# Kernel tuning notes

Measured on AMD Instinct MI355X. Metric: run time of the kernel, lower is better.

## Reference

```python
import jax, jax.numpy as jnp
import numpy as np

B, S_ENC, T_DEC, I, H = 1024, 49, 25, 76, 2048  # S_ENC = source_seq_len - 1


def setup_inputs() -> dict:
    key = jax.random.key(0)
    ks = jax.random.split(key, 6)
    sc = 0.02
    return {
        "encoder_inputs": jax.random.normal(ks[0], (B, S_ENC, I), jnp.float32),
        "decoder_inputs": jax.random.normal(ks[1], (B, T_DEC, I), jnp.float32),
        "W_ih": jax.random.normal(ks[2], (3 * H, I), jnp.float32) * sc,
        "W_hh": jax.random.normal(ks[3], (3 * H, H), jnp.float32) * sc,
        "b_ih": jnp.zeros((3 * H,), jnp.float32),
        "b_hh": jnp.zeros((3 * H,), jnp.float32),
        "fc_w": jax.random.normal(ks[4], (I, H), jnp.float32) * sc,
        "fc_b": jnp.zeros((I,), jnp.float32),
    }


def gru_cell(x, h, W_ih, W_hh, b_ih, b_hh):
    # PyTorch GRUCell: gates stacked [r; z; n] along first axis of weights.
    gi = x @ W_ih.T + b_ih  # [B, 3H]
    gh = h @ W_hh.T + b_hh  # [B, 3H]
    i_r, i_z, i_n = jnp.split(gi, 3, axis=-1)
    h_r, h_z, h_n = jnp.split(gh, 3, axis=-1)
    r = jax.nn.sigmoid(i_r + h_r)
    z = jax.nn.sigmoid(i_z + h_z)
    n = jnp.tanh(i_n + r * h_n)
    return (1.0 - z) * n + z * h


def reference(encoder_inputs, decoder_inputs, W_ih, W_hh, b_ih, b_hh, fc_w, fc_b):
    # Dropout p=0.0 (and eval mode) -> identity; omitted.
    h0 = jnp.zeros((encoder_inputs.shape[0], H), encoder_inputs.dtype)
    enc = jnp.swapaxes(encoder_inputs, 0, 1)  # [S_ENC, B, I]

    def enc_step(h, x):
        return gru_cell(x, h, W_ih, W_hh, b_ih, b_hh), None

    h, _ = jax.lax.scan(enc_step, h0, enc)

    # Sampling-based decoding: only decoder_inputs[:, 0] is consumed; every
    # later step feeds back the previous output. Each step's input is detached.
    prev0 = decoder_inputs[:, 0, :]

    def dec_step(carry, _):
        h, prev = carry
        inp = jax.lax.stop_gradient(prev)  # inp.detach() in the torch code
        h_new = gru_cell(inp, h, W_ih, W_hh, b_ih, b_hh)
        out = inp + h_new @ fc_w.T + fc_b  # residual over fc1 projection
        return (h_new, out), out

    _, outs = jax.lax.scan(dec_step, (h, prev0), None, length=T_DEC)
    return jnp.swapaxes(outs, 0, 1)  # [B, T_DEC, I]
```

## Files before the change

kernel.cpp:

```cpp
#include <hip/hip_runtime.h>
#include <cstdint>
#include <cstddef>

#define DI __device__ __forceinline__

typedef __bf16 bf16x8 __attribute__((ext_vector_type(8)));
typedef float  f32x4  __attribute__((ext_vector_type(4)));
typedef unsigned short ushort_t;

constexpr int BATCH = 1024;
constexpr int HID   = 2048;
constexpr int IN    = 76;
constexpr int SENC  = 49;
constexpr int TDEC  = 25;
constexpr int KX    = 128;
constexpr int KP    = KX + HID;
constexpr int BK    = 128;
constexpr int KTT   = KP / BK;
constexpr int OSTR  = TDEC * IN;

DI unsigned short f2bf(float f) {
  union { float f; unsigned u; } v; v.f = f;
  unsigned u = v.u;
  return (unsigned short)((u + 0x7fffu + ((u >> 16) & 1u)) >> 16);
}

DI float bf2f(unsigned short h) {
  union { unsigned u; float f; } v; v.u = ((unsigned)h) << 16;
  return v.f;
}

DI f32x4 mfma16(bf16x8 a, bf16x8 b, f32x4 c) {
  return __builtin_amdgcn_mfma_f32_16x16x32_bf16(a, b, c, 0, 0, 0);
}

DI void gload_lds16(const void* g, void* l) {
  __builtin_amdgcn_global_load_lds((const __attribute__((address_space(1))) void*)g,
                                   (__attribute__((address_space(3))) void*)l,
                                   16, 0, 0);
}

DI float sigmoidf_(float x) { return 1.0f / (1.0f + __expf(-x)); }
DI float tanhf_(float x)    { return 1.0f - 2.0f / (1.0f + __expf(2.0f * x)); }


__global__ void pack_W(const float* __restrict__ Wih, const float* __restrict__ Whh,
                       ushort_t* __restrict__ Wp) {
  int idx = blockIdx.x * 256 + threadIdx.x;
  if (idx >= 6144 * KP) return;
  int n = idx / KP;
  int k = idx - n * KP;
  float v = 0.f;
  if (k < IN)        v = Wih[(size_t)n * IN + k];
  else if (k >= KX)  v = Whh[(size_t)n * HID + (k - KX)];
  Wp[idx] = f2bf(v);
}

__global__ void pack_xe(const float* __restrict__ enc, ushort_t* __restrict__ xe) {
  int idx = blockIdx.x * 256 + threadIdx.x;
  if (idx >= SENC * BATCH * KX) return;
  int t = idx >> 17;
  int rem = idx & 131071;
  int b = rem >> 7, k = rem & 127;
  float v = (k < IN) ? enc[(size_t)b * (SENC * IN) + t * IN + k] : 0.f;
  xe[idx] = f2bf(v);
}

__global__ void pack_xd0(const float* __restrict__ dec, ushort_t* __restrict__ xd) {
  int idx = blockIdx.x * 256 + threadIdx.x;
  if (idx >= BATCH * KX) return;
  int b = idx >> 7, k = idx & 127;
  float v = (k < IN) ? dec[(size_t)b * OSTR + k] : 0.f;
  xd[idx] = f2bf(v);
}

__global__ void pack_fc(const float* __restrict__ fcw, ushort_t* __restrict__ Wfc) {
  int idx = blockIdx.x * 256 + threadIdx.x;
  if (idx >= 80 * HID) return;
  int n = idx >> 11, k = idx & 2047;
  float v = (n < IN) ? fcw[(size_t)n * HID + k] : 0.f;
  Wfc[idx] = f2bf(v);
}

__global__ __launch_bounds__(512, 2) void gru_step_kernel(
    const ushort_t* __restrict__ x,
    const ushort_t* __restrict__ hbp,
    const ushort_t* __restrict__ Wp,
    const float*    __restrict__ b_ih,
    const float*    __restrict__ b_hh,
    ushort_t*       __restrict__ hbn)
{
  __shared__ ushort_t lds[2][(128 + 192) * BK];

  const int tid  = threadIdx.x;
  const int lane = tid & 63;
  const int wid  = tid >> 6;
  const int bid  = blockIdx.x;
  const int n_grp = (bid & 7) + 8 * (bid >> 6);
  const int m_grp = (bid >> 3) & 7;
  const int row0  = m_grp * 128;
  const int col0  = n_grp * 64;
  const int wm = wid >> 1, wn = wid & 1;

  const f32x4 Z4 = {0.f, 0.f, 0.f, 0.f};
  f32x4 accr[2][2], accz[2][2], accin[2][2], accN[2][2];
  #pragma unroll
  for (int a = 0; a < 2; ++a)
    #pragma unroll
    for (int b = 0; b < 2; ++b) { accr[a][b] = Z4; accz[a][b] = Z4; accin[a][b] = Z4; accN[a][b] = Z4; }

  const int l15 = lane & 15;
  const int lhi = lane >> 4;

  auto stage = [&](int buf, int kt) {
    const ushort_t* asrc; int astr, ak0;
    if (kt == 0) { asrc = x;   astr = KX;  ak0 = 0; }
    else         { asrc = hbp; astr = HID; ak0 = (kt - 1) * BK; }
    ushort_t* Lb = &lds[buf][0];
    #pragma unroll
    for (int c = 0; c < 4; ++c) {
      const int chunk = wid * 4 + c;
      const int rl = chunk * 4 + lhi;
      const int swz = ((l15 ^ (((chunk & 3) << 2) + lhi)) << 3);
      const ushort_t* g = asrc + (size_t)(row0 + rl) * astr + ak0 + swz;
      gload_lds16(g, Lb + chunk * 512);
    }
    const int wk0 = kt * BK;
    #pragma unroll
    for (int c = 0; c < 6; ++c) {
      const int chunk = wid * 6 + c;
      const int brow = chunk * 4 + lhi;
      const int gg = brow >> 6, wi = brow & 63;
      const int swz = ((l15 ^ (((chunk & 3) << 2) + lhi)) << 3);
      const ushort_t* g = Wp + (size_t)(gg * HID + col0 + wi) * KP + wk0 + swz;
      gload_lds16(g, Lb + 128 * BK + chunk * 512);
    }
  };

  auto readFrags = [&](const ushort_t* base, int ks, bf16x8 af[2], bf16x8 bg[3][2]) {
    const int el = (((ks << 2) + lhi) ^ l15) << 3;
    #pragma unroll
    for (int fm = 0; fm < 2; ++fm)
      af[fm] = *reinterpret_cast<const bf16x8*>(&base[(wm * 32 + fm * 16 + l15) * BK + el]);
    #pragma unroll
    for (int g = 0; g < 3; ++g)
      #pragma unroll
      for (int fn = 0; fn < 2; ++fn)
        bg[g][fn] = *reinterpret_cast<const bf16x8*>(
            &base[128 * BK + (g * 64 + wn * 32 + fn * 16 + l15) * BK + el]);
  };

  auto burst = [&](bf16x8 af[2], bf16x8 bg[3][2]) {
    __builtin_amdgcn_s_setprio(1);
    #pragma unroll
    for (int fm = 0; fm < 2; ++fm)
      #pragma unroll
      for (int fn = 0; fn < 2; ++fn) {
        accr[fm][fn] = mfma16(af[fm], bg[0][fn], accr[fm][fn]);
        accz[fm][fn] = mfma16(af[fm], bg[1][fn], accz[fm][fn]);
        accN[fm][fn] = mfma16(af[fm], bg[2][fn], accN[fm][fn]);
      }
    __builtin_amdgcn_s_setprio(0);
  };

  bf16x8 afA[2], bgA[3][2];
  bf16x8 afB[2], bgB[3][2];

  stage(0, 0);
  asm volatile("s_waitcnt vmcnt(0)" ::: "memory");
  __builtin_amdgcn_s_barrier();
  readFrags(&lds[0][0], 0, afA, bgA);

  for (int kt = 0; kt < KTT; ++kt) {
    const ushort_t* base = &lds[kt & 1][0];
    if (kt + 1 < KTT) stage((kt + 1) & 1, kt + 1);

    readFrags(base, 1, afB, bgB);  burst(afA, bgA);
    readFrags(base, 2, afA, bgA);  burst(afB, bgB);
    readFrags(base, 3, afB, bgB);  burst(afA, bgA);
    burst(afB, bgB);

    if (kt == 0) {
      #pragma unroll
      for (int a = 0; a < 2; ++a)
        #pragma unroll
        for (int b = 0; b < 2; ++b) { accin[a][b] = accN[a][b]; accN[a][b] = Z4; }
    }

    if (kt + 1 < KTT) {
      asm volatile("s_waitcnt vmcnt(0)" ::: "memory");
      __builtin_amdgcn_s_barrier();
      readFrags(&lds[(kt + 1) & 1][0], 0, afA, bgA);
    }
  }

  const int lqb = lhi * 4;
  #pragma unroll
  for (int fn = 0; fn < 2; ++fn) {
    const int j = col0 + wn * 32 + fn * 16 + l15;
    const float br  = b_ih[j] + b_hh[j];
    const float bz  = b_ih[HID + j] + b_hh[HID + j];
    const float bin = b_ih[2 * HID + j];
    const float bhn = b_hh[2 * HID + j];
    #pragma unroll
    for (int fm = 0; fm < 2; ++fm) {
      #pragma unroll
      for (int q = 0; q < 4; ++q) {
        const int row = row0 + wm * 32 + fm * 16 + lqb + q;
        const size_t off = (size_t)row * HID + j;
        const float hp = bf2f(hbp[off]);
        const float rr = sigmoidf_(accr[fm][fn][q] + br);
        const float zz = sigmoidf_(accz[fm][fn][q] + bz);
        const float nn = tanhf_(accin[fm][fn][q] + bin + rr * (accN[fm][fn][q] + bhn));
        const float hv = (1.0f - zz) * nn + zz * hp;
        hbn[off] = f2bf(hv);
      }
    }
  }
}

__global__ __launch_bounds__(256) void fc_kernel(
    const ushort_t* __restrict__ hb,
    const ushort_t* __restrict__ Wfc,
    const float*    __restrict__ fc_b,
    const float*    __restrict__ prev,
    float*          __restrict__ outp,
    ushort_t*       __restrict__ xd)
{
  __shared__ float red[4][16][80];
  const int tid = threadIdx.x, lane = tid & 63, wid = tid >> 6;
  const int r0 = blockIdx.x * 16;
  const int lr = lane & 15, lk = (lane >> 4) * 8;
  const f32x4 Z4 = {0.f, 0.f, 0.f, 0.f};
  f32x4 acc[5];
  #pragma unroll
  for (int f = 0; f < 5; ++f) acc[f] = Z4;
  const int kbase = wid * 512;
  #pragma unroll
  for (int ks = 0; ks < 16; ++ks) {
    const int k = kbase + ks * 32 + lk;
    bf16x8 a = *reinterpret_cast<const bf16x8*>(&hb[(size_t)(r0 + lr) * HID + k]);
    #pragma unroll
    for (int f = 0; f < 5; ++f) {
      bf16x8 b = *reinterpret_cast<const bf16x8*>(&Wfc[(size_t)(f * 16 + lr) * HID + k]);
      acc[f] = mfma16(a, b, acc[f]);
    }
  }
  #pragma unroll
  for (int f = 0; f < 5; ++f)
    #pragma unroll
    for (int q = 0; q < 4; ++q)
      red[wid][(lane >> 4) * 4 + q][f * 16 + lr] = acc[f][q];
  __syncthreads();

  const int rowi = tid >> 4;
  const int j0   = (tid & 15) * 8;
  const int b_   = r0 + rowi;
  #pragma unroll
  for (int jj = 0; jj < 8; ++jj) {
    const int j = j0 + jj;
    float ov = 0.f;
    if (j < IN) {
      float s = red[0][rowi][j] + red[1][rowi][j] + red[2][rowi][j] + red[3][rowi][j];
      ov = prev[(size_t)b_ * OSTR + j] + fc_b[j] + s;
      outp[(size_t)b_ * OSTR + j] = ov;
    }
    xd[b_ * KX + j] = f2bf(j < IN ? ov : 0.f);
  }
}

extern "C" void kernel_launch(void* const* d_in, const int* in_sizes, int n_in,
                              void* d_out, int out_size, void* d_ws, size_t ws_size,
                              hipStream_t stream) {
  const float* enc = (const float*)d_in[0];
  const float* dec = (const float*)d_in[1];
  const float* Wih = (const float*)d_in[2];
  const float* Whh = (const float*)d_in[3];
  const float* bih = (const float*)d_in[4];
  const float* bhh = (const float*)d_in[5];
  const float* fcw = (const float*)d_in[6];
  const float* fcb = (const float*)d_in[7];
  float* out = (float*)d_out;

  char* ws = (char*)d_ws;
  ushort_t* Wp  = (ushort_t*)ws;  ws += (size_t)6144 * KP * 2;
  ushort_t* xe  = (ushort_t*)ws;  ws += (size_t)SENC * BATCH * KX * 2;
  ushort_t* xd  = (ushort_t*)ws;  ws += (size_t)BATCH * KX * 2;
  ushort_t* Wfc = (ushort_t*)ws;  ws += (size_t)80 * HID * 2;
  ushort_t* hb0 = (ushort_t*)ws;  ws += (size_t)BATCH * HID * 2;
  ushort_t* hb1 = (ushort_t*)ws;  ws += (size_t)BATCH * HID * 2;
  ushort_t* hbp[2] = {hb0, hb1};

  pack_W  <<<(6144 * KP + 255) / 256, 256, 0, stream>>>(Wih, Whh, Wp);
  pack_xe <<<(SENC * BATCH * KX + 255) / 256, 256, 0, stream>>>(enc, xe);
  pack_xd0<<<(BATCH * KX + 255) / 256, 256, 0, stream>>>(dec, xd);
  pack_fc <<<(80 * HID + 255) / 256, 256, 0, stream>>>(fcw, Wfc);
  hipMemsetAsync(hb0, 0, (size_t)BATCH * HID * 2, stream);

  for (int s = 0; s < SENC + TDEC; ++s) {
    const ushort_t* xsrc = (s < SENC) ? (xe + (size_t)s * BATCH * KX) : xd;
    gru_step_kernel<<<256, 512, 0, stream>>>(xsrc, hbp[s & 1], Wp, bih, bhh,
                                             hbp[(s + 1) & 1]);
    if (s >= SENC) {
      const int t = s - SENC;
      const float* prev = (t == 0) ? dec : (out + (size_t)(t - 1) * IN);
      fc_kernel<<<64, 256, 0, stream>>>(hbp[(s + 1) & 1], Wfc, fcb, prev,
                                        out + (size_t)t * IN, xd);
    }
  }
}
```

Measured before the change: 2.631 ms.

## Halve GRU block threads, double per-wave tile, deepen LDS fragment pipeline

Each GRU step block now runs 256 threads instead of 512, so every wave computes a 64x64 output sub-tile (four M fragments) rather than 32x64. The main loop is restructured into a four-stage register pipeline (A/B/C/D fragment sets), with the x-projection tile peeled out as a prologue and the next tile's global-to-LDS load issued between fragment reads. s_setprio around the MFMA bursts is removed. Intent is more MFMA work per LDS fragment read and better latency hiding. The cost is much higher register pressure (64 accumulator vectors plus four fragment sets) and fewer waves per block for hiding memory latency.

```diff
diff --git a/kernel.cpp b/kernel.cpp
--- a/kernel.cpp
+++ b/kernel.cpp
@@ -82,7 +82,7 @@
   Wfc[idx] = f2bf(v);
 }
 
-__global__ __launch_bounds__(512, 2) void gru_step_kernel(
+__global__ __launch_bounds__(256, 1) void gru_step_kernel(
     const ushort_t* __restrict__ x,
     const ushort_t* __restrict__ hbp,
     const ushort_t* __restrict__ Wp,
@@ -103,32 +103,50 @@
   const int wm = wid >> 1, wn = wid & 1;
 
   const f32x4 Z4 = {0.f, 0.f, 0.f, 0.f};
-  f32x4 accr[2][2], accz[2][2], accin[2][2], accN[2][2];
-  #pragma unroll
-  for (int a = 0; a < 2; ++a)
-    #pragma unroll
-    for (int b = 0; b < 2; ++b) { accr[a][b] = Z4; accz[a][b] = Z4; accin[a][b] = Z4; accN[a][b] = Z4; }
+  f32x4 accr[4][2], accz[4][2], accN[4][2], accin[4][2];
+  #pragma unroll
+  for (int a = 0; a < 4; ++a)
+    #pragma unroll
+    for (int b = 0; b < 2; ++b) { accr[a][b] = Z4; accz[a][b] = Z4; accN[a][b] = Z4; accin[a][b] = Z4; }
 
   const int l15 = lane & 15;
   const int lhi = lane >> 4;
 
-  auto stage = [&](int buf, int kt) {
-    const ushort_t* asrc; int astr, ak0;
-    if (kt == 0) { asrc = x;   astr = KX;  ak0 = 0; }
-    else         { asrc = hbp; astr = HID; ak0 = (kt - 1) * BK; }
-    ushort_t* Lb = &lds[buf][0];
-    #pragma unroll
-    for (int c = 0; c < 4; ++c) {
-      const int chunk = wid * 4 + c;
+  auto stageX = [&]() {
+    ushort_t* Lb = &lds[0][0];
+    #pragma unroll
+    for (int c = 0; c < 8; ++c) {
+      const int chunk = wid * 8 + c;
       const int rl = chunk * 4 + lhi;
       const int swz = ((l15 ^ (((chunk & 3) << 2) + lhi)) << 3);
-      const ushort_t* g = asrc + (size_t)(row0 + rl) * astr + ak0 + swz;
+      const ushort_t* g = x + (size_t)(row0 + rl) * KX + swz;
       gload_lds16(g, Lb + chunk * 512);
     }
+    #pragma unroll
+    for (int c = 0; c < 12; ++c) {
+      const int chunk = wid * 12 + c;
+      const int brow = chunk * 4 + lhi;
+      const int gg = brow >> 6, wi = brow & 63;
+      const int swz = ((l15 ^ (((chunk & 3) << 2) + lhi)) << 3);
+      const ushort_t* g = Wp + (size_t)(gg * HID + col0 + wi) * KP + swz;
+      gload_lds16(g, Lb + 128 * BK + chunk * 512);
+    }
+  };
+  auto stageH = [&](int buf, int kt) {
+    const int ak0 = (kt - 1) * BK;
     const int wk0 = kt * BK;
-    #pragma unroll
-    for (int c = 0; c < 6; ++c) {
-      const int chunk = wid * 6 + c;
+    ushort_t* Lb = &lds[buf][0];
+    #pragma unroll
+    for (int c = 0; c < 8; ++c) {
+      const int chunk = wid * 8 + c;
+      const int rl = chunk * 4 + lhi;
+      const int swz = ((l15 ^ (((chunk & 3) << 2) + lhi)) << 3);
+      const ushort_t* g = hbp + (size_t)(row0 + rl) * HID + ak0 + swz;
+      gload_lds16(g, Lb + chunk * 512);
+    }
+    #pragma unroll
+    for (int c = 0; c < 12; ++c) {
+      const int chunk = wid * 12 + c;
       const int brow = chunk * 4 + lhi;
       const int gg = brow >> 6, wi = brow & 63;
       const int swz = ((l15 ^ (((chunk & 3) << 2) + lhi)) << 3);
@@ -137,81 +155,91 @@
     }
   };
 
-  auto readFrags = [&](const ushort_t* base, int ks, bf16x8 af[2], bf16x8 bg[3][2]) {
+  auto readFrags = [&](const ushort_t* base, int ks, bf16x8 af[4], bf16x8 bg[3][2]) {
     const int el = (((ks << 2) + lhi) ^ l15) << 3;
     #pragma unroll
-    for (int fm = 0; fm < 2; ++fm)
-      af[fm] = *reinterpret_cast<const bf16x8*>(&base[(wm * 32 + fm * 16 + l15) * BK + el]);
+    for (int fm = 0; fm < 4; ++fm)
+      af[fm] = *reinterpret_cast<const bf16x8*>(&base[(wm * 64 + fm * 16 + l15) * BK + el]);
     #pragma unroll
     for (int g = 0; g < 3; ++g)
       #pragma unroll
-      for (int fn = 0; fn < 2; ++fn)
-        bg[g][fn] = *reinterpret_cast<const bf16x8*>(
-            &base[128 * BK + (g * 64 + wn * 32 + fn * 16 + l15) * BK + el]);
+      for (int fnh = 0; fnh < 2; ++fnh)
+        bg[g][fnh] = *reinterpret_cast<const bf16x8*>(
+            &base[128 * BK + (g * 64 + wn * 32 + fnh * 16 + l15) * BK + el]);
   };
 
-  auto burst = [&](bf16x8 af[2], bf16x8 bg[3][2]) {
-    __builtin_amdgcn_s_setprio(1);
-    #pragma unroll
-    for (int fm = 0; fm < 2; ++fm)
+  auto burst = [&](bf16x8 af[4], bf16x8 bg[3][2]) {
+    #pragma unroll
+    for (int fm = 0; fm < 4; ++fm)
       #pragma unroll
-      for (int fn = 0; fn < 2; ++fn) {
-        accr[fm][fn] = mfma16(af[fm], bg[0][fn], accr[fm][fn]);
-        accz[fm][fn] = mfma16(af[fm], bg[1][fn], accz[fm][fn]);
-        accN[fm][fn] = mfma16(af[fm], bg[2][fn], accN[fm][fn]);
+      for (int fnh = 0; fnh < 2; ++fnh) {
+        accr[fm][fnh] = mfma16(af[fm], bg[0][fnh], accr[fm][fnh]);
+        accz[fm][fnh] = mfma16(af[fm], bg[1][fnh], accz[fm][fnh]);
+        accN[fm][fnh] = mfma16(af[fm], bg[2][fnh], accN[fm][fnh]);
       }
-    __builtin_amdgcn_s_setprio(0);
   };
 
-  bf16x8 afA[2], bgA[3][2];
-  bf16x8 afB[2], bgB[3][2];
-
-  stage(0, 0);
+  bf16x8 afA[4], bgA[3][2], afB[4], bgB[3][2];
+  bf16x8 afC[4], bgC[3][2], afD[4], bgD[3][2];
+
+  stageX();
   asm volatile("s_waitcnt vmcnt(0)" ::: "memory");
   __builtin_amdgcn_s_barrier();
   readFrags(&lds[0][0], 0, afA, bgA);
-
-  for (int kt = 0; kt < KTT; ++kt) {
+  readFrags(&lds[0][0], 1, afB, bgB);
+  stageH(1, 1);
+  readFrags(&lds[0][0], 2, afC, bgC);
+  burst(afA, bgA);
+  readFrags(&lds[0][0], 3, afD, bgD);
+  burst(afB, bgB);
+  asm volatile("s_waitcnt lgkmcnt(0)" ::: "memory");
+  asm volatile("s_waitcnt vmcnt(0)" ::: "memory");
+  __builtin_amdgcn_s_barrier();
+  burst(afC, bgC);
+
+  for (int kt = 1; kt < KTT; ++kt) {
     const ushort_t* base = &lds[kt & 1][0];
-    if (kt + 1 < KTT) stage((kt + 1) & 1, kt + 1);
-
-    readFrags(base, 1, afB, bgB);  burst(afA, bgA);
-    readFrags(base, 2, afA, bgA);  burst(afB, bgB);
-    readFrags(base, 3, afB, bgB);  burst(afA, bgA);
-    burst(afB, bgB);
-
-    if (kt == 0) {
+    readFrags(base, 0, afA, bgA);
+    readFrags(base, 1, afB, bgB);
+    if (kt + 1 < KTT) stageH((kt + 1) & 1, kt + 1);
+    burst(afD, bgD);
+    if (kt == 1) {
       #pragma unroll
-      for (int a = 0; a < 2; ++a)
+      for (int a = 0; a < 4; ++a)
         #pragma unroll
         for (int b = 0; b < 2; ++b) { accin[a][b] = accN[a][b]; accN[a][b] = Z4; }
     }
-
+    readFrags(base, 2, afC, bgC);
+    burst(afA, bgA);
+    readFrags(base, 3, afD, bgD);
+    burst(afB, bgB);
+    asm volatile("s_waitcnt lgkmcnt(0)" ::: "memory");
     if (kt + 1 < KTT) {
       asm volatile("s_waitcnt vmcnt(0)" ::: "memory");
       __builtin_amdgcn_s_barrier();
-      readFrags(&lds[(kt + 1) & 1][0], 0, afA, bgA);
-    }
-  }
+    }
+    burst(afC, bgC);
+  }
+  burst(afD, bgD);
 
   const int lqb = lhi * 4;
   #pragma unroll
-  for (int fn = 0; fn < 2; ++fn) {
-    const int j = col0 + wn * 32 + fn * 16 + l15;
+  for (int fnh = 0; fnh < 2; ++fnh) {
+    const int j = col0 + wn * 32 + fnh * 16 + l15;
     const float br  = b_ih[j] + b_hh[j];
     const float bz  = b_ih[HID + j] + b_hh[HID + j];
     const float bin = b_ih[2 * HID + j];
     const float bhn = b_hh[2 * HID + j];
     #pragma unroll
-    for (int fm = 0; fm < 2; ++fm) {
+    for (int fm = 0; fm < 4; ++fm) {
       #pragma unroll
       for (int q = 0; q < 4; ++q) {
-        const int row = row0 + wm * 32 + fm * 16 + lqb + q;
+        const int row = row0 + wm * 64 + fm * 16 + lqb + q;
         const size_t off = (size_t)row * HID + j;
         const float hp = bf2f(hbp[off]);
-        const float rr = sigmoidf_(accr[fm][fn][q] + br);
-        const float zz = sigmoidf_(accz[fm][fn][q] + bz);
-        const float nn = tanhf_(accin[fm][fn][q] + bin + rr * (accN[fm][fn][q] + bhn));
+        const float rr = sigmoidf_(accr[fm][fnh][q] + br);
+        const float zz = sigmoidf_(accz[fm][fnh][q] + bz);
+        const float nn = tanhf_(accin[fm][fnh][q] + bin + rr * (accN[fm][fnh][q] + bhn));
         const float hv = (1.0f - zz) * nn + zz * hp;
         hbn[off] = f2bf(hv);
       }
@@ -299,7 +327,7 @@
 
   for (int s = 0; s < SENC + TDEC; ++s) {
     const ushort_t* xsrc = (s < SENC) ? (xe + (size_t)s * BATCH * KX) : xd;
-    gru_step_kernel<<<256, 512, 0, stream>>>(xsrc, hbp[s & 1], Wp, bih, bhh,
+    gru_step_kernel<<<256, 256, 0, stream>>>(xsrc, hbp[s & 1], Wp, bih, bhh,
                                              hbp[(s + 1) & 1]);
     if (s >= SENC) {
       const int t = s - SENC;
```

New measurement: 3.401 ms. +29.3%, slower.

## Load GEMM A operand directly to registers and triple-buffer weights in LDS

Applied to the files above, without the earlier changes.

The x/h activation tiles (A operand) are no longer staged through LDS. Each wave now loads its A fragments straight from global memory into registers, prefetching the next k-tile during the current MFMA bursts. LDS now holds only the weight (B) tiles, in three buffers that are staged two tiles ahead, and a partial vmcnt wait replaces the full drain. This is meant to cut LDS traffic and barrier stalls. The costs are uncoalesced direct global reads for A, and an LDS buffer being refilled without a barrier guarding reads still in flight in slower waves.

```diff
diff --git a/kernel.cpp b/kernel.cpp
--- a/kernel.cpp
+++ b/kernel.cpp
@@ -90,7 +90,7 @@
     const float*    __restrict__ b_hh,
     ushort_t*       __restrict__ hbn)
 {
-  __shared__ ushort_t lds[2][(128 + 192) * BK];
+  __shared__ ushort_t lds[3][192 * BK];
 
   const int tid  = threadIdx.x;
   const int lane = tid & 63;
@@ -102,29 +102,17 @@
   const int col0  = n_grp * 64;
   const int wm = wid >> 1, wn = wid & 1;
 
-  const f32x4 Z4 = {0.f, 0.f, 0.f, 0.f};
-  f32x4 accr[2][2], accz[2][2], accin[2][2], accN[2][2];
-  #pragma unroll
-  for (int a = 0; a < 2; ++a)
-    #pragma unroll
-    for (int b = 0; b < 2; ++b) { accr[a][b] = Z4; accz[a][b] = Z4; accin[a][b] = Z4; accN[a][b] = Z4; }
-
   const int l15 = lane & 15;
   const int lhi = lane >> 4;
 
-  auto stage = [&](int buf, int kt) {
-    const ushort_t* asrc; int astr, ak0;
-    if (kt == 0) { asrc = x;   astr = KX;  ak0 = 0; }
-    else         { asrc = hbp; astr = HID; ak0 = (kt - 1) * BK; }
-    ushort_t* Lb = &lds[buf][0];
-    #pragma unroll
-    for (int c = 0; c < 4; ++c) {
-      const int chunk = wid * 4 + c;
-      const int rl = chunk * 4 + lhi;
-      const int swz = ((l15 ^ (((chunk & 3) << 2) + lhi)) << 3);
-      const ushort_t* g = asrc + (size_t)(row0 + rl) * astr + ak0 + swz;
-      gload_lds16(g, Lb + chunk * 512);
-    }
+  const f32x4 Z4 = {0.f, 0.f, 0.f, 0.f};
+  f32x4 accr[2][2], accz[2][2], accN[2][2], accin[2][2];
+  #pragma unroll
+  for (int a = 0; a < 2; ++a)
+    #pragma unroll
+    for (int b = 0; b < 2; ++b) { accr[a][b] = Z4; accz[a][b] = Z4; accN[a][b] = Z4; accin[a][b] = Z4; }
+
+  auto stageB = [&](ushort_t* Lb, int kt) {
     const int wk0 = kt * BK;
     #pragma unroll
     for (int c = 0; c < 6; ++c) {
@@ -132,22 +120,33 @@
       const int brow = chunk * 4 + lhi;
       const int gg = brow >> 6, wi = brow & 63;
       const int swz = ((l15 ^ (((chunk & 3) << 2) + lhi)) << 3);
-      const ushort_t* g = Wp + (size_t)(gg * HID + col0 + wi) * KP + wk0 + swz;
-      gload_lds16(g, Lb + 128 * BK + chunk * 512);
-    }
-  };
-
-  auto readFrags = [&](const ushort_t* base, int ks, bf16x8 af[2], bf16x8 bg[3][2]) {
+      gload_lds16(Wp + (size_t)(gg * HID + col0 + wi) * KP + wk0 + swz,
+                  Lb + chunk * 512);
+    }
+  };
+
+  auto readB = [&](const ushort_t* Lb, int ks, bf16x8 bg[3][2]) {
     const int el = (((ks << 2) + lhi) ^ l15) << 3;
-    #pragma unroll
-    for (int fm = 0; fm < 2; ++fm)
-      af[fm] = *reinterpret_cast<const bf16x8*>(&base[(wm * 32 + fm * 16 + l15) * BK + el]);
     #pragma unroll
     for (int g = 0; g < 3; ++g)
       #pragma unroll
       for (int fn = 0; fn < 2; ++fn)
         bg[g][fn] = *reinterpret_cast<const bf16x8*>(
-            &base[128 * BK + (g * 64 + wn * 32 + fn * 16 + l15) * BK + el]);
+            &Lb[(g * 64 + wn * 32 + fn * 16 + l15) * BK + el]);
+  };
+
+  auto loadAx = [&](int ks, bf16x8 af[2]) {
+    #pragma unroll
+    for (int fm = 0; fm < 2; ++fm)
+      af[fm] = *reinterpret_cast<const bf16x8*>(
+          &x[(size_t)(row0 + wm * 32 + fm * 16 + l15) * KX + ks * 32 + lhi * 8]);
+  };
+  auto loadAh = [&](int kt, int ks, bf16x8 af[2]) {
+    const int k = (kt - 1) * BK + ks * 32 + lhi * 8;
+    #pragma unroll
+    for (int fm = 0; fm < 2; ++fm)
+      af[fm] = *reinterpret_cast<const bf16x8*>(
+          &hbp[(size_t)(row0 + wm * 32 + fm * 16 + l15) * HID + k]);
   };
 
   auto burst = [&](bf16x8 af[2], bf16x8 bg[3][2]) {
@@ -163,34 +162,37 @@
     __builtin_amdgcn_s_setprio(0);
   };
 
-  bf16x8 afA[2], bgA[3][2];
-  bf16x8 afB[2], bgB[3][2];
-
-  stage(0, 0);
-  asm volatile("s_waitcnt vmcnt(0)" ::: "memory");
-  __builtin_amdgcn_s_barrier();
-  readFrags(&lds[0][0], 0, afA, bgA);
+  bf16x8 aS0[2], aS1[2], aS2[2], aS3[2];
+  bf16x8 bSa[3][2], bSb[3][2];
+
+  stageB(&lds[0][0], 0);
+  stageB(&lds[1][0], 1);
+  loadAx(0, aS0); loadAx(1, aS1); loadAx(2, aS2); loadAx(3, aS3);
 
   for (int kt = 0; kt < KTT; ++kt) {
-    const ushort_t* base = &lds[kt & 1][0];
-    if (kt + 1 < KTT) stage((kt + 1) & 1, kt + 1);
-
-    readFrags(base, 1, afB, bgB);  burst(afA, bgA);
-    readFrags(base, 2, afA, bgA);  burst(afB, bgB);
-    readFrags(base, 3, afB, bgB);  burst(afA, bgA);
-    burst(afB, bgB);
+    ushort_t* cur = &lds[kt % 3][0];
+    if (kt + 2 < KTT) stageB(&lds[(kt + 2) % 3][0], kt + 2);
+    asm volatile("s_waitcnt vmcnt(14)" ::: "memory");
+    __builtin_amdgcn_s_barrier();
+
+    readB(cur, 0, bSa);
+    readB(cur, 1, bSb);
+    burst(aS0, bSa);
+    if (kt + 1 < KTT) loadAh(kt + 1, 0, aS0);
+    readB(cur, 2, bSa);
+    burst(aS1, bSb);
+    if (kt + 1 < KTT) loadAh(kt + 1, 1, aS1);
+    readB(cur, 3, bSb);
+    burst(aS2, bSa);
+    if (kt + 1 < KTT) loadAh(kt + 1, 2, aS2);
+    burst(aS3, bSb);
+    if (kt + 1 < KTT) loadAh(kt + 1, 3, aS3);
 
     if (kt == 0) {
       #pragma unroll
       for (int a = 0; a < 2; ++a)
         #pragma unroll
         for (int b = 0; b < 2; ++b) { accin[a][b] = accN[a][b]; accN[a][b] = Z4; }
-    }
-
-    if (kt + 1 < KTT) {
-      asm volatile("s_waitcnt vmcnt(0)" ::: "memory");
-      __builtin_amdgcn_s_barrier();
-      readFrags(&lds[(kt + 1) & 1][0], 0, afA, bgA);
     }
   }
 
```

Result: slower. 3.510 ms (+33.4%).
